# Kernel tuning notes

Measured on AMD Instinct MI355X. Metric: run time of the kernel, lower is better.

## Reference

```python
import jax, jax.numpy as jnp
import numpy as np

N_HEAD = 12
N_EMBED = 768

def setup_inputs() -> dict:
    key = jax.random.key(0)
    ks = jax.random.split(key, 5)
    B, T, C = 8, 1024, N_EMBED
    s_in = 1.0 / np.sqrt(C)
    s3 = 1.0 / np.sqrt(3 * C)
    return {
        "x": jax.random.normal(ks[0], (B, T, C), dtype=jnp.float32),
        "W_qkv": jax.random.normal(ks[1], (C, 3 * C), dtype=jnp.float32) * s_in,
        "b_qkv": jnp.zeros((3 * C,), dtype=jnp.float32),
        "W_out": jax.random.normal(ks[2], (C, C), dtype=jnp.float32) * s_in,
        "b_out": jnp.zeros((C,), dtype=jnp.float32),
    }

def reference(x, W_qkv, b_qkv, W_out, b_out):
    B, T, C = x.shape
    H = N_HEAD
    d_k = C // H
    qkv = x @ W_qkv + b_qkv  # [B,T,3C]
    q, k, v = jnp.split(qkv, 3, axis=-1)
    # [B,H,T,d]
    q = q.reshape(B, T, H, d_k).transpose(0, 2, 1, 3)
    k = k.reshape(B, T, H, d_k).transpose(0, 2, 1, 3)
    v = v.reshape(B, T, H, d_k).transpose(0, 2, 1, 3)
    logits = jnp.einsum('bhqd,bhkd->bhqk', q, k) * (d_k ** -0.5)
    causal = jnp.tril(jnp.ones((T, T), dtype=bool))
    logits = jnp.where(causal, logits, -jnp.inf)
    scores = jax.nn.softmax(logits, axis=-1)
    out = jnp.einsum('bhqk,bhkd->bhqd', scores, v)
    out = out.transpose(0, 2, 1, 3).reshape(B, T, C)
    return out @ W_out + b_out
```

## Files before the change

kernel.cpp:

```cpp
#include <hip/hip_runtime.h>
#include <stdint.h>

#define B_ 8
#define T_ 1024
#define C_ 768
#define H_ 12
#define DK 64
#define BT (B_*T_)
#define NQKV (3*C_)

typedef unsigned short u16;
typedef __bf16 bf16x8 __attribute__((ext_vector_type(8)));
typedef __bf16 bf16x4 __attribute__((ext_vector_type(4)));
typedef float  f32x4  __attribute__((ext_vector_type(4)));

typedef const __attribute__((address_space(1))) void gvoid_t;
typedef __attribute__((address_space(3))) void lvoid_t;

#define SBARRIER()  asm volatile("s_barrier" ::: "memory")
#define SWAITCNT(s) asm volatile("s_waitcnt " s ::: "memory")

__device__ __forceinline__ void gl_lds16(const void* g, void* l) {
    __builtin_amdgcn_global_load_lds((gvoid_t*)g, (lvoid_t*)l, 16, 0, 0);
}

__device__ __forceinline__ u16 f2b(float f) {
    union { float f; unsigned int u; } v; v.f = f;
    unsigned int u = v.u;
    return (u16)((u + 0x7fffu + ((u >> 16) & 1u)) >> 16);
}

__device__ __forceinline__ f32x4 mfma16(bf16x8 a, bf16x8 b, f32x4 c) {
    return __builtin_amdgcn_mfma_f32_16x16x32_bf16(a, b, c, 0, 0, 0);
}

__global__ __launch_bounds__(256)
void k_prep(const float* __restrict__ x, u16* __restrict__ xb,
            const float* __restrict__ wqkv, u16* __restrict__ wqkvT,
            const float* __restrict__ wout, u16* __restrict__ woutT)
{
    __shared__ u16 tile[32][34];
    const int bid = blockIdx.x;
    const int tid = threadIdx.x;
    if (bid < 6144) {
        int i = bid * 256 + tid;
        float4 f = ((const float4*)x)[i];
        uint2 o;
        o.x = (unsigned)f2b(f.x) | ((unsigned)f2b(f.y) << 16);
        o.y = (unsigned)f2b(f.z) | ((unsigned)f2b(f.w) << 16);
        ((uint2*)xb)[i] = o;
        return;
    }
    const float* w; u16* wt; int K, N, n0, k0;
    if (bid < 6144 + 1728) {
        int idx = bid - 6144;
        w = wqkv; wt = wqkvT; K = C_; N = NQKV;
        n0 = (idx % 72) * 32; k0 = (idx / 72) * 32;
    } else {
        int idx = bid - 7872;
        w = wout; wt = woutT; K = C_; N = C_;
        n0 = (idx % 24) * 32; k0 = (idx / 24) * 32;
    }
    const int tx = tid & 31, ty = tid >> 5;
    #pragma unroll
    for (int i = 0; i < 4; i++)
        tile[ty + i * 8][tx] = f2b(w[(size_t)(k0 + ty + i * 8) * N + n0 + tx]);
    __syncthreads();
    #pragma unroll
    for (int i = 0; i < 4; i++)
        wt[(size_t)(n0 + ty + i * 8) * K + k0 + tx] = tile[tx][ty + i * 8];
}

__global__ __launch_bounds__(256, 2)
void k_gemm_qkv(const u16* __restrict__ A, const u16* __restrict__ Bt,
                const float* __restrict__ bias,
                u16* __restrict__ qo, u16* __restrict__ ko, u16* __restrict__ vto)
{
    const int K = C_;
    __shared__ u16 As[3][128 * 32];
    __shared__ u16 Bs[3][288 * 32];
    const int tid  = threadIdx.x;
    const int lane = tid & 63;
    const int w    = tid >> 6;
    const int quad = lane >> 4;
    const int col  = lane & 15;

    const int id   = blockIdx.x + gridDim.x * blockIdx.y;
    const int xcd  = id & 7;
    const int slot = id >> 3;
    const int m0   = (xcd * 8 + (slot & 7)) * 128;
    const int n0   = (slot >> 3) * 96;

    const int wm   = w * 32;

    f32x4 zero4 = {0.f, 0.f, 0.f, 0.f};
    f32x4 acc[2][18];
    #pragma unroll
    for (int i = 0; i < 2; i++)
        #pragma unroll
        for (int j = 0; j < 18; j++) acc[i][j] = zero4;

    const int sr  = tid >> 2;
    const int scc = ((tid & 3) ^ ((sr >> 1) & 3)) * 8;
    const u16* gA = A  + (size_t)(m0 + sr) * K + scc;
    const u16* gB = Bt + (size_t)(n0 + sr) * K + scc;

    const int NIT = K >> 5;

    #define STAGE(kt, bufi)                                                               \
        do {                                                                              \
            gl_lds16(gA + (kt),                  (char*)As[bufi] + w * 1024);             \
            gl_lds16(gA + (size_t)64 * K + (kt), (char*)As[bufi] + 4096 + w * 1024);      \
            _Pragma("unroll")                                                             \
            for (int s = 0; s < 3; s++) {                                                 \
                const u16* gBs = gB + (size_t)(s * C_) * K;                               \
                gl_lds16(gBs + (kt), (char*)Bs[bufi] + s * 6144 + w * 1024);              \
                if (w < 2)                                                                \
                    gl_lds16(gBs + (size_t)64 * K + (kt),                                 \
                             (char*)Bs[bufi] + s * 6144 + 4096 + w * 1024);               \
            }                                                                             \
        } while (0)

    STAGE(0, 0);
    STAGE(32, 1);
    int cur = 0;
    for (int it = 0; it < NIT; ++it) {
        if (it + 1 < NIT) {
            if (w < 2) { SWAITCNT("vmcnt(8)"); } else { SWAITCNT("vmcnt(5)"); }
        } else {
            SWAITCNT("vmcnt(0)");
        }
        SBARRIER();
        if (it + 2 < NIT) {
            int b2 = cur + 2; if (b2 >= 3) b2 -= 3;
            STAGE((it + 2) << 5, b2);
        }

        const u16* Ab = As[cur];
        const u16* Bb = Bs[cur];
        bf16x8 af[2];
        #pragma unroll
        for (int mt = 0; mt < 2; mt++) {
            int row = wm + mt * 16 + col;
            af[mt] = *(const bf16x8*)&Ab[row * 32 + ((quad ^ ((row >> 1) & 3)) * 8)];
        }
        #pragma unroll
        for (int nt = 0; nt < 18; nt++) {
            int row = nt * 16 + col;
            bf16x8 bfr = *(const bf16x8*)&Bb[row * 32 + ((quad ^ ((row >> 1) & 3)) * 8)];
            acc[0][nt] = mfma16(af[0], bfr, acc[0][nt]);
            acc[1][nt] = mfma16(af[1], bfr, acc[1][nt]);
        }

        cur = (cur == 2) ? 0 : cur + 1;
    }
    #undef STAGE

    #pragma unroll
    for (int mt = 0; mt < 2; mt++) {
        #pragma unroll
        for (int nt = 0; nt < 18; nt++) {
            const int sec = nt / 6;
            const int cc  = n0 + (nt - sec * 6) * 16 + col;
            const int h   = cc >> 6;
            const int d   = cc & 63;
            #pragma unroll
            for (int r = 0; r < 4; r++) {
                int m = m0 + wm + mt * 16 + quad * 4 + r;
                int b = m >> 10;
                int t = m & 1023;
                int bh = b * H_ + h;
                float v = acc[mt][nt][r] + bias[sec * C_ + cc];
                u16 bv = f2b(v);
                if (sec == 0)      qo [((size_t)bh * T_ + t) * DK + d] = bv;
                else if (sec == 1) ko [((size_t)bh * T_ + t) * DK + d] = bv;
                else               vto[((size_t)bh * DK + d) * T_ + t] = bv;
            }
        }
    }
}

__global__ __launch_bounds__(256, 2)
void k_gemm_out(const u16* __restrict__ A, const u16* __restrict__ Bt,
                const float* __restrict__ bias, float* __restrict__ outf)
{
    const int K = C_, N = C_;
    __shared__ u16 As[2][2][128 * 32];
    __shared__ u16 Bs[2][2][96 * 32];
    const int tid  = threadIdx.x;
    const int lane = tid & 63;
    const int w    = tid >> 6;
    const int quad = lane >> 4;
    const int col  = lane & 15;

    const int id   = blockIdx.x;
    const int xcd  = id & 7;
    const int slot = id >> 3;
    const int m0   = (xcd * 8 + (slot & 7)) * 128;
    const int n0   = (slot >> 3) * 96;

    const int wm   = w * 32;

    f32x4 zero4 = {0.f, 0.f, 0.f, 0.f};
    f32x4 acc[2][6];
    #pragma unroll
    for (int i = 0; i < 2; i++)
        #pragma unroll
        for (int j = 0; j < 6; j++) acc[i][j] = zero4;

    const int sr  = tid >> 2;
    const int scc = ((tid & 3) ^ ((sr >> 1) & 3)) * 8;
    const u16* gA = A  + (size_t)(m0 + sr) * K + scc;
    const u16* gB = Bt + (size_t)(n0 + sr) * K + scc;

    const int NT64 = K >> 6;

    #define SUB(kt, bufi, subi)                                                           \
        do {                                                                              \
            gl_lds16(gA + (kt),                  (char*)As[bufi][subi] + w * 1024);       \
            gl_lds16(gA + (size_t)64 * K + (kt), (char*)As[bufi][subi] + 4096 + w * 1024);\
            gl_lds16(gB + (kt),                  (char*)Bs[bufi][subi] + w * 1024);       \
            if (w < 2)                                                                    \
                gl_lds16(gB + (size_t)64 * K + (kt), (char*)Bs[bufi][subi] + 4096 + w * 1024);\
        } while (0)
    #define STAGE(t, bufi)  do { SUB(((t) << 6), bufi, 0); SUB(((t) << 6) + 32, bufi, 1); } while (0)

    STAGE(0, 0);
    for (int it = 0; it < NT64; ++it) {
        const int cur = it & 1;
        SWAITCNT("vmcnt(0)");
        SBARRIER();
        if (it + 1 < NT64)
            STAGE(it + 1, cur ^ 1);

        #pragma unroll
        for (int kk = 0; kk < 2; ++kk) {
            const u16* Ab = As[cur][kk];
            const u16* Bb = Bs[cur][kk];
            bf16x8 af[2], bfr[6];
            #pragma unroll
            for (int mt = 0; mt < 2; mt++) {
                int row = wm + mt * 16 + col;
                af[mt] = *(const bf16x8*)&Ab[row * 32 + ((quad ^ ((row >> 1) & 3)) * 8)];
            }
            #pragma unroll
            for (int nt = 0; nt < 6; nt++) {
                int row = nt * 16 + col;
                bfr[nt] = *(const bf16x8*)&Bb[row * 32 + ((quad ^ ((row >> 1) & 3)) * 8)];
            }
            #pragma unroll
            for (int mt = 0; mt < 2; mt++)
                #pragma unroll
                for (int nt = 0; nt < 6; nt++)
                    acc[mt][nt] = mfma16(af[mt], bfr[nt], acc[mt][nt]);
        }
    }
    #undef STAGE
    #undef SUB

    #pragma unroll
    for (int mt = 0; mt < 2; mt++) {
        #pragma unroll
        for (int nt = 0; nt < 6; nt++) {
            #pragma unroll
            for (int r = 0; r < 4; r++) {
                int m = m0 + wm + mt * 16 + quad * 4 + r;
                int n = n0 + nt * 16 + col;
                outf[(size_t)m * N + n] = acc[mt][nt][r] + bias[n];
            }
        }
    }
}

#define PSTRIDE 72

__device__ __forceinline__ bf16x8 ld_sw(const u16* base, int row, int half,
                                        int quad, int c7) {
    return *(const bf16x8*)(base + row * DK + (((half * 4 + quad) ^ c7) * 8));
}

template <bool MASK>
__device__ __forceinline__ void attn_chunk(
    const u16* Ks, const u16* Vs, __bf16* pbuf,
    const bf16x8 (&qf)[2][2], bf16x8 ones,
    int kv0, int qw, int quad, int col,
    f32x4 (&oacc)[2][4], f32x4 (&lacc)[2])
{
    const int c7 = col & 7;
    f32x4 zero4 = {0.f, 0.f, 0.f, 0.f};
    f32x4 st[2][4];
    #pragma unroll
    for (int g = 0; g < 4; g++) {
        bf16x8 klo = ld_sw(Ks, g * 16 + col, 0, quad, c7);
        bf16x8 khi = ld_sw(Ks, g * 16 + col, 1, quad, c7);
        st[0][g] = mfma16(khi, qf[0][1], mfma16(klo, qf[0][0], zero4));
        st[1][g] = mfma16(khi, qf[1][1], mfma16(klo, qf[1][0], zero4));
    }
    const float scl = 0.18033688f;
    #pragma unroll
    for (int s = 0; s < 2; s++) {
        __bf16* pb = pbuf + s * 16 * PSTRIDE + col * PSTRIDE;
        #pragma unroll
        for (int g = 0; g < 4; g++) {
            bf16x4 pp;
            #pragma unroll
            for (int r = 0; r < 4; r++) {
                float p = __builtin_amdgcn_exp2f(st[s][g][r] * scl - 12.0f);
                if (MASK) {
                    int kv = kv0 + g * 16 + quad * 4 + r;
                    if (kv > qw + s * 16 + col) p = 0.f;
                }
                pp[r] = (__bf16)p;
            }
            *(bf16x4*)(pb + g * 16 + quad * 4) = pp;
        }
    }
    SWAITCNT("lgkmcnt(0)");
    bf16x8 pf[2][2];
    #pragma unroll
    for (int s = 0; s < 2; s++) {
        const __bf16* pb = pbuf + s * 16 * PSTRIDE + col * PSTRIDE;
        pf[s][0] = *(const bf16x8*)(pb + quad * 8);
        pf[s][1] = *(const bf16x8*)(pb + 32 + quad * 8);
        lacc[s] = mfma16(pf[s][1], ones, mfma16(pf[s][0], ones, lacc[s]));
    }
    #pragma unroll
    for (int dt = 0; dt < 4; dt++) {
        bf16x8 vlo = ld_sw(Vs, dt * 16 + col, 0, quad, c7);
        bf16x8 vhi = ld_sw(Vs, dt * 16 + col, 1, quad, c7);
        #pragma unroll
        for (int s = 0; s < 2; s++)
            oacc[s][dt] = mfma16(pf[s][1], vhi, mfma16(pf[s][0], vlo, oacc[s][dt]));
    }
}

__global__ __launch_bounds__(256, 3)
void k_attn(const u16* __restrict__ Q, const u16* __restrict__ Kf,
            const u16* __restrict__ Vt, u16* __restrict__ Of)
{
    __shared__ u16 Ks[2][64 * DK];
    __shared__ u16 Vs[2][64 * DK];
    __shared__ __bf16 Plds[4][32 * PSTRIDE];
    const int bh   = blockIdx.x;
    const int b    = bh / H_;
    const int h    = bh - b * H_;
    const int tid  = threadIdx.x;
    const int lane = tid & 63;
    const int w    = tid >> 6;
    const int quad = lane >> 4;
    const int col  = lane & 15;
    const int ty   = 7 - (int)blockIdx.y;
    const int nch  = 2 * ty + 2;
    const int qw   = ty * 128 + w * 32;
    __bf16* pbuf = Plds[w];

    const u16* Qb = Q  + (size_t)bh * T_ * DK;
    const u16* Kb = Kf + (size_t)bh * T_ * DK;
    const u16* Vb = Vt + (size_t)bh * DK * T_;

    int sG0 = tid, sG1 = 256 + tid;
    int sr0 = sG0 >> 3, sg0 = (sG0 & 7) ^ (sr0 & 7);
    int sr1 = sG1 >> 3, sg1 = (sG1 & 7) ^ (sr1 & 7);

    bf16x8 qf[2][2];
    #pragma unroll
    for (int s = 0; s < 2; s++) {
        const u16* qp = Qb + (size_t)(qw + s * 16 + col) * DK;
        qf[s][0] = *(const bf16x8*)(qp + quad * 8);
        qf[s][1] = *(const bf16x8*)(qp + 32 + quad * 8);
    }

    bf16x8 ones;
    #pragma unroll
    for (int i = 0; i < 8; i++) ((u16*)&ones)[i] = 0x3F80;

    f32x4 zero4 = {0.f, 0.f, 0.f, 0.f};
    f32x4 oacc[2][4];
    f32x4 lacc[2] = {zero4, zero4};
    #pragma unroll
    for (int s = 0; s < 2; s++)
        #pragma unroll
        for (int dt = 0; dt < 4; dt++) oacc[s][dt] = zero4;

    #define ASTAGE(c, bufi)                                                            \
        do {                                                                           \
            int kvs = (c) * 64;                                                        \
            gl_lds16(Kb + (size_t)(kvs + sr0) * DK + sg0 * 8, (char*)Ks[bufi] + w * 1024);        \
            gl_lds16(Kb + (size_t)(kvs + sr1) * DK + sg1 * 8, (char*)Ks[bufi] + 4096 + w * 1024); \
            gl_lds16(Vb + (size_t)sr0 * T_ + kvs + sg0 * 8,   (char*)Vs[bufi] + w * 1024);        \
            gl_lds16(Vb + (size_t)sr1 * T_ + kvs + sg1 * 8,   (char*)Vs[bufi] + 4096 + w * 1024); \
        } while (0)

    ASTAGE(0, 0);
    #pragma unroll 1
    for (int c = 0; c < nch; ++c) {
        const int cur = c & 1;
        SWAITCNT("vmcnt(0)");
        SBARRIER();
        if (c + 1 < nch) {
            ASTAGE(c + 1, cur ^ 1);
        }

        const int kv0 = c * 64;
        if (kv0 <= qw + 31) {
            if (kv0 + 63 <= qw)
                attn_chunk<false>(Ks[cur], Vs[cur], pbuf, qf, ones, kv0, qw, quad, col, oacc, lacc);
            else
                attn_chunk<true>(Ks[cur], Vs[cur], pbuf, qf, ones, kv0, qw, quad, col, oacc, lacc);
        }
    }
    #undef ASTAGE

    #pragma unroll
    for (int s = 0; s < 2; s++) {
        #pragma unroll
        for (int r = 0; r < 4; r++) {
            float inv = 1.f / lacc[s][r];
            int t = qw + s * 16 + quad * 4 + r;
            u16* op = Of + ((size_t)(b * T_ + t)) * C_ + h * DK;
            #pragma unroll
            for (int dt = 0; dt < 4; dt++) op[dt * 16 + col] = f2b(oacc[s][dt][r] * inv);
        }
    }
}

extern "C" void kernel_launch(void* const* d_in, const int* in_sizes, int n_in,
                              void* d_out, int out_size, void* d_ws, size_t ws_size,
                              hipStream_t stream) {
    const float* x    = (const float*)d_in[0];
    const float* Wqkv = (const float*)d_in[1];
    const float* bqkv = (const float*)d_in[2];
    const float* Wout = (const float*)d_in[3];
    const float* bout = (const float*)d_in[4];
    float* out = (float*)d_out;

    char* ws = (char*)d_ws;
    u16* xb    = (u16*)(ws);
    u16* wqkvT = (u16*)(ws + 12582912);
    u16* woutT = (u16*)(ws + 16121856);
    u16* qw    = (u16*)(ws + 17301504);
    u16* kw    = (u16*)(ws + 29884416);
    u16* vtw   = (u16*)(ws + 42467328);
    u16* aw    = (u16*)(ws + 55050240);

    k_prep<<<8448, 256, 0, stream>>>(x, xb, Wqkv, wqkvT, Wout, woutT);

    k_gemm_qkv<<<dim3(8, BT / 128), 256, 0, stream>>>(
        xb, wqkvT, bqkv, qw, kw, vtw);

    k_attn<<<dim3(B_ * H_, 8), 256, 0, stream>>>(qw, kw, vtw, aw);

    k_gemm_out<<<512, 256, 0, stream>>>(aw, woutT, bout, out);
}
```

Measured before the change: 172.6 us.

## Load K/V fragments directly from global memory instead of LDS staging

Removes the double-buffered LDS staging of K and V tiles, along with the per-chunk barriers and async global-to-LDS copies, in the attention kernel. Each wave now reads its MFMA K and V fragments straight from global memory, relying on L1/L2 caching. This drops LDS use and block-level synchronisation, which may raise occupancy. In exchange, the four waves now each fetch the same K/V data redundantly, and the loads are not prefetched ahead of use, so latency is exposed.

```diff
diff --git a/kernel.cpp b/kernel.cpp
--- a/kernel.cpp
+++ b/kernel.cpp
@@ -274,25 +274,20 @@
 
 #define PSTRIDE 72
 
-__device__ __forceinline__ bf16x8 ld_sw(const u16* base, int row, int half,
-                                        int quad, int c7) {
-    return *(const bf16x8*)(base + row * DK + (((half * 4 + quad) ^ c7) * 8));
-}
-
 template <bool MASK>
 __device__ __forceinline__ void attn_chunk(
-    const u16* Ks, const u16* Vs, __bf16* pbuf,
+    const u16* __restrict__ Kb, const u16* __restrict__ Vb, __bf16* pbuf,
     const bf16x8 (&qf)[2][2], bf16x8 ones,
     int kv0, int qw, int quad, int col,
     f32x4 (&oacc)[2][4], f32x4 (&lacc)[2])
 {
-    const int c7 = col & 7;
     f32x4 zero4 = {0.f, 0.f, 0.f, 0.f};
     f32x4 st[2][4];
     #pragma unroll
     for (int g = 0; g < 4; g++) {
-        bf16x8 klo = ld_sw(Ks, g * 16 + col, 0, quad, c7);
-        bf16x8 khi = ld_sw(Ks, g * 16 + col, 1, quad, c7);
+        const u16* kp = Kb + (size_t)(kv0 + g * 16 + col) * DK + quad * 8;
+        bf16x8 klo = *(const bf16x8*)(kp);
+        bf16x8 khi = *(const bf16x8*)(kp + 32);
         st[0][g] = mfma16(khi, qf[0][1], mfma16(klo, qf[0][0], zero4));
         st[1][g] = mfma16(khi, qf[1][1], mfma16(klo, qf[1][0], zero4));
     }
@@ -326,8 +321,9 @@
     }
     #pragma unroll
     for (int dt = 0; dt < 4; dt++) {
-        bf16x8 vlo = ld_sw(Vs, dt * 16 + col, 0, quad, c7);
-        bf16x8 vhi = ld_sw(Vs, dt * 16 + col, 1, quad, c7);
+        const u16* vp = Vb + (size_t)(dt * 16 + col) * T_ + kv0 + quad * 8;
+        bf16x8 vlo = *(const bf16x8*)(vp);
+        bf16x8 vhi = *(const bf16x8*)(vp + 32);
         #pragma unroll
         for (int s = 0; s < 2; s++)
             oacc[s][dt] = mfma16(pf[s][1], vhi, mfma16(pf[s][0], vlo, oacc[s][dt]));
@@ -338,8 +334,6 @@
 void k_attn(const u16* __restrict__ Q, const u16* __restrict__ Kf,
             const u16* __restrict__ Vt, u16* __restrict__ Of)
 {
-    __shared__ u16 Ks[2][64 * DK];
-    __shared__ u16 Vs[2][64 * DK];
     __shared__ __bf16 Plds[4][32 * PSTRIDE];
     const int bh   = blockIdx.x;
     const int b    = bh / H_;
@@ -358,10 +352,6 @@
     const u16* Kb = Kf + (size_t)bh * T_ * DK;
     const u16* Vb = Vt + (size_t)bh * DK * T_;
 
-    int sG0 = tid, sG1 = 256 + tid;
-    int sr0 = sG0 >> 3, sg0 = (sG0 & 7) ^ (sr0 & 7);
-    int sr1 = sG1 >> 3, sg1 = (sG1 & 7) ^ (sr1 & 7);
-
     bf16x8 qf[2][2];
     #pragma unroll
     for (int s = 0; s < 2; s++) {
@@ -382,34 +372,16 @@
         #pragma unroll
         for (int dt = 0; dt < 4; dt++) oacc[s][dt] = zero4;
 
-    #define ASTAGE(c, bufi)                                                            \
-        do {                                                                           \
-            int kvs = (c) * 64;                                                        \
-            gl_lds16(Kb + (size_t)(kvs + sr0) * DK + sg0 * 8, (char*)Ks[bufi] + w * 1024);        \
-            gl_lds16(Kb + (size_t)(kvs + sr1) * DK + sg1 * 8, (char*)Ks[bufi] + 4096 + w * 1024); \
-            gl_lds16(Vb + (size_t)sr0 * T_ + kvs + sg0 * 8,   (char*)Vs[bufi] + w * 1024);        \
-            gl_lds16(Vb + (size_t)sr1 * T_ + kvs + sg1 * 8,   (char*)Vs[bufi] + 4096 + w * 1024); \
-        } while (0)
-
-    ASTAGE(0, 0);
     #pragma unroll 1
     for (int c = 0; c < nch; ++c) {
-        const int cur = c & 1;
-        SWAITCNT("vmcnt(0)");
-        SBARRIER();
-        if (c + 1 < nch) {
-            ASTAGE(c + 1, cur ^ 1);
-        }
-
         const int kv0 = c * 64;
         if (kv0 <= qw + 31) {
             if (kv0 + 63 <= qw)
-                attn_chunk<false>(Ks[cur], Vs[cur], pbuf, qf, ones, kv0, qw, quad, col, oacc, lacc);
+                attn_chunk<false>(Kb, Vb, pbuf, qf, ones, kv0, qw, quad, col, oacc, lacc);
             else
-                attn_chunk<true>(Ks[cur], Vs[cur], pbuf, qf, ones, kv0, qw, quad, col, oacc, lacc);
-        }
-    }
-    #undef ASTAGE
+                attn_chunk<true>(Kb, Vb, pbuf, qf, ones, kv0, qw, quad, col, oacc, lacc);
+        }
+    }
 
     #pragma unroll
     for (int s = 0; s < 2; s++) {
```

Measured after the change: 211.4 us. 22.4% more time.
